# Optimization experiments

Hardware: AMD Instinct MI355X
Metric: run time of the kernel (lower is better)

The kernel has to match this reference:

```python
import jax, jax.numpy as jnp
import numpy as np
import math

H = 16        # num_heads
HD = 64       # head_dim


def get_slopes(n):
    def pow2(n):
        start = 2 ** (-2 ** (-(math.log2(n) - 3)))
        return [start * start ** i for i in range(n)]
    if math.log2(n).is_integer():
        return pow2(n)
    c = 2 ** math.floor(math.log2(n))
    return pow2(c) + get_slopes(2 * c)[0::2][: n - c]


def setup_inputs() -> dict:
    key = jax.random.key(0)
    ks = jax.random.split(key, 6)
    b, n, d = 2, 2048, 1024
    s = 1.0 / math.sqrt(d)
    return {
        "x": jax.random.normal(ks[0], (b, n, d), jnp.float32),
        "Wq": jax.random.normal(ks[1], (d, d), jnp.float32) * s,
        "Wk": jax.random.normal(ks[2], (d, d), jnp.float32) * s,
        "Wv": jax.random.normal(ks[3], (d, d), jnp.float32) * s,
        "Wo": jax.random.normal(ks[4], (d, d), jnp.float32) * s,
        "bo": jnp.zeros((d,), jnp.float32),
    }


def reference(x, Wq, Wk, Wv, Wo, bo):
    b, n, d = x.shape
    # project and split heads: [b, H, n, HD]
    def heads(w):
        return (x @ w).reshape(b, n, H, HD).transpose(0, 2, 1, 3)
    q, k, v = heads(Wq), heads(Wk), heads(Wv)

    scores = jnp.einsum("bhqd,bhkd->bhqk", q, k)  # [b,H,n,n]
    pos = jnp.arange(n)
    dist = jnp.abs(pos[None, :] - pos[:, None]).astype(scores.dtype)  # [n,n]
    slopes = jnp.asarray(get_slopes(H), dtype=scores.dtype)
    scores = scores - slopes[:, None, None] * dist  # alibi subtracted BEFORE scaling (as in source)
    causal = pos[None, :] > pos[:, None]            # upper triangle masked
    scores = jnp.where(causal, -jnp.inf, scores)
    attn = jax.nn.softmax(scores / math.sqrt(HD), axis=-1)
    ctx = jnp.einsum("bhqk,bhkd->bhqd", attn, v)
    ctx = ctx.transpose(0, 2, 1, 3).reshape(b, n, d)
    return ctx @ Wo + bo
```

## Files before the change

### kernel.cpp

```cpp
#include <hip/hip_runtime.h>
#include <hip/hip_bf16.h>
#include <stdint.h>

#define NH 16
#define HDIM 64
#define NB 2
#define NSEQ 2048
#define DM 1024
#define MROWS (NB * NSEQ)

typedef __attribute__((ext_vector_type(8))) short bf16x8;
typedef __attribute__((ext_vector_type(4))) float f32x4;

#define MFMA32(a, b, c) __builtin_amdgcn_mfma_f32_16x16x32_bf16(a, b, c, 0, 0, 0)

static __device__ __forceinline__ unsigned short f2bf(float f) {
    union { float f; unsigned u; } v;
    v.f = f;
    unsigned r = v.u + 0x7fffu + ((v.u >> 16) & 1u);
    return (unsigned short)(r >> 16);
}

static __device__ __forceinline__ unsigned pack2bf(float a, float b) {
#if __has_builtin(__builtin_amdgcn_cvt_pk_bf16_f32)
    typedef __attribute__((ext_vector_type(2))) __bf16 bf2_t;
    union { bf2_t v; unsigned u; } c;
    c.v = __builtin_amdgcn_cvt_pk_bf16_f32(a, b);
    return c.u;
#else
    return (unsigned)f2bf(a) | ((unsigned)f2bf(b) << 16);
#endif
}

static __device__ __forceinline__ float fexp2(float x) {
#if __has_builtin(__builtin_amdgcn_exp2f)
    return __builtin_amdgcn_exp2f(x);
#else
    return exp2f(x);
#endif
}

typedef __attribute__((address_space(1))) void* gas_ptr;
typedef __attribute__((address_space(3))) void* las_ptr;

static __device__ __forceinline__ void load16_lds(const void* g, void* l) {
    __builtin_amdgcn_global_load_lds((gas_ptr)(uintptr_t)g, (las_ptr)(uintptr_t)l,
                                     16, 0, 0);
}

__global__ __launch_bounds__(256) void convert_kernel(
    const float* __restrict__ x,
    const float* __restrict__ wq, const float* __restrict__ wk,
    const float* __restrict__ wv, const float* __restrict__ wo,
    unsigned short* __restrict__ xb,
    unsigned short* __restrict__ wqkvt,
    unsigned short* __restrict__ wot)
{
    __shared__ unsigned short Ts[64][66];
    int t = threadIdx.x;
    int bx = blockIdx.x;
    if (bx < 1024) {
        const float4* xs = (const float4*)x + (long)bx * 1024;
        unsigned short* xd = xb + (long)bx * 4096;
#pragma unroll
        for (int i = 0; i < 4; i++) {
            float4 v = xs[i * 256 + t];
            ushort4 o;
            o.x = f2bf(v.x); o.y = f2bf(v.y); o.z = f2bf(v.z); o.w = f2bf(v.w);
            *(ushort4*)(xd + (i * 256 + t) * 4) = o;
        }
        return;
    }
    int wi = bx - 1024;
    int wsel = wi >> 8;
    int tile = wi & 255;
    int k0 = (tile >> 4) * 64, c0 = (tile & 15) * 64;
    const float* w = (wsel == 0) ? wq : (wsel == 1) ? wk : (wsel == 2) ? wv : wo;
    int lr = t >> 6, lc = t & 63;
#pragma unroll
    for (int rr = 0; rr < 16; rr++) {
        int row = rr * 4 + lr;
        Ts[row][lc] = f2bf(w[(long)(k0 + row) * DM + c0 + lc]);
    }
    __syncthreads();
    unsigned short* dst = (wsel == 3) ? wot : (wqkvt + (long)wsel * DM * DM);
#pragma unroll
    for (int rr = 0; rr < 16; rr++) {
        int crow = rr * 4 + lr;
        dst[(long)(c0 + crow) * DM + k0 + lc] = Ts[lc][crow];
    }
}

static __device__ __forceinline__ void gemm_tile_128(
    const unsigned short* __restrict__ A, const unsigned short* __restrict__ Bt,
    int m0, int n0, unsigned short* As, unsigned short* Bs, f32x4 (&acc)[4][4])
{
    int t = threadIdx.x;
    int lane = t & 63;
    int wave = t >> 6;
    int l16 = lane & 15, quad = lane >> 4;
    int wm = wave >> 1, wn = wave & 1;

    int b0 = t, b1 = t + 256;
    int row0 = b0 >> 2, g0 = (b0 & 3) ^ ((row0 >> 1) & 3);
    int row1 = b1 >> 2, g1 = (b1 & 3) ^ ((row1 >> 1) & 3);
    const char* ga0 = (const char*)(A + (long)(m0 + row0) * DM) + g0 * 16;
    const char* ga1 = (const char*)(A + (long)(m0 + row1) * DM) + g1 * 16;
    const char* gb0 = (const char*)(Bt + (long)(n0 + row0) * DM) + g0 * 16;
    const char* gb1 = (const char*)(Bt + (long)(n0 + row1) * DM) + g1 * 16;
    char* sa0 = (char*)As + t * 16;
    char* sa1 = (char*)As + t * 16 + 4096;
    char* sb0 = (char*)Bs + t * 16;
    char* sb1 = (char*)Bs + t * 16 + 4096;

    int sread = quad ^ ((l16 >> 1) & 3);
    const unsigned short* fa = As + (wm * 64 + l16) * 32 + sread * 8;
    const unsigned short* fb = Bs + (wn * 64 + l16) * 32 + sread * 8;

    for (int kk = 0; kk < DM; kk += 32) {
        load16_lds(ga0 + kk * 2, sa0);
        load16_lds(ga1 + kk * 2, sa1);
        load16_lds(gb0 + kk * 2, sb0);
        load16_lds(gb1 + kk * 2, sb1);
        __syncthreads();
        bf16x8 af[4], bf[4];
#pragma unroll
        for (int r = 0; r < 4; r++) af[r] = *(const bf16x8*)(fa + r * 16 * 32);
#pragma unroll
        for (int c = 0; c < 4; c++) bf[c] = *(const bf16x8*)(fb + c * 16 * 32);
#pragma unroll
        for (int r = 0; r < 4; r++)
#pragma unroll
            for (int c = 0; c < 4; c++)
                acc[r][c] = MFMA32(af[r], bf[c], acc[r][c]);
        __syncthreads();
    }
}

__global__ __launch_bounds__(256) void qkv_gemm_kernel(
    const unsigned short* __restrict__ A,
    const unsigned short* __restrict__ Bt,
    unsigned short* __restrict__ Qo, unsigned short* __restrict__ Ko,
    unsigned short* __restrict__ Vt)
{
    __shared__ unsigned short As[128 * 32];
    __shared__ unsigned short Bs[128 * 32];
    __shared__ unsigned short Tw[4][16][72];

    f32x4 acc[4][4] = {};
    int m0 = blockIdx.y * 128, n0 = blockIdx.x * 128;
    gemm_tile_128(A, Bt, m0, n0, As, Bs, acc);

    int t = threadIdx.x, wave = t >> 6, lane = t & 63;
    int l16 = lane & 15, quad = lane >> 4;
    int wm = wave >> 1, wn = wave & 1;
    int rg0 = m0 + wm * 64;
    int cg0 = n0 + wn * 64;
    int z = cg0 >> 10;
    int b_ = rg0 >> 11;
    int nb0 = rg0 & (NSEQ - 1);
    int h = (cg0 & 1023) >> 6;
    long bh = (long)(b_ * NH + h);

    if (z < 2) {
        unsigned short* dst = (z == 0 ? Qo : Ko) + bh * NSEQ * HDIM;
#pragma unroll
        for (int r = 0; r < 4; r++)
#pragma unroll
            for (int reg = 0; reg < 4; reg++) {
                long rowb = (long)(nb0 + r * 16 + quad * 4 + reg) * HDIM;
#pragma unroll
                for (int c = 0; c < 4; c++)
                    dst[rowb + c * 16 + l16] = f2bf(acc[r][c][reg]);
            }
    } else {
        unsigned short* dst = Vt + bh * HDIM * NSEQ;
#pragma unroll
        for (int c = 0; c < 4; c++) {
#pragma unroll
            for (int r = 0; r < 4; r++) {
                ushort4 u;
                u.x = f2bf(acc[r][c][0]); u.y = f2bf(acc[r][c][1]);
                u.z = f2bf(acc[r][c][2]); u.w = f2bf(acc[r][c][3]);
                *(ushort4*)&Tw[wave][l16][r * 16 + quad * 4] = u;
            }
#pragma unroll
            for (int j = 0; j < 4; j++) {
                int lrow = j * 4 + quad;
                ushort4 u = *(const ushort4*)&Tw[wave][lrow][l16 * 4];
                *(ushort4*)(dst + (long)(c * 16 + lrow) * NSEQ + nb0 + l16 * 4) = u;
            }
        }
    }
}

static __device__ __forceinline__ void softmax_fixed(
    f32x4* s, bool mask, int qb, int kb, float sc2, float mrow,
    f32x4& l_vec, unsigned pbu[2][4], int l16, int quad)
{
    if (mask) {
        int fdm = qb + l16 - kb - quad * 4;
#pragma unroll
        for (int tt = 0; tt < 4; tt++)
#pragma unroll
            for (int r = 0; r < 4; r++)
                if (tt * 16 + r > fdm) s[tt][r] = -3e38f;
    }
    f32x4 e[4];
#pragma unroll
    for (int tt = 0; tt < 4; tt++)
#pragma unroll
        for (int r = 0; r < 4; r++)
            e[tt][r] = fexp2(s[tt][r] * sc2 - mrow);
#pragma unroll
    for (int r = 0; r < 4; r++)
        l_vec[r] += (e[0][r] + e[1][r]) + (e[2][r] + e[3][r]);

#pragma unroll
    for (int p = 0; p < 2; p++) {
        pbu[p][0] = pack2bf(e[2 * p][0],     e[2 * p][1]);
        pbu[p][1] = pack2bf(e[2 * p][2],     e[2 * p][3]);
        pbu[p][2] = pack2bf(e[2 * p + 1][0], e[2 * p + 1][1]);
        pbu[p][3] = pack2bf(e[2 * p + 1][2], e[2 * p + 1][3]);
    }
}

__global__ __launch_bounds__(512) void attn_kernel(
    const unsigned short* __restrict__ Q,
    const unsigned short* __restrict__ K,
    const unsigned short* __restrict__ Vt,
    unsigned short* __restrict__ ctx)
{
    __shared__ unsigned short KV[2][8192];

    int t = threadIdx.x, w = t >> 6, lane = t & 63;
    int l16 = lane & 15, quad = lane >> 4;
    int r7 = l16 & 7;
    int bh = blockIdx.x;
    int b_ = bh >> 4, h = bh & 15;
    int pr = blockIdx.y;
    int t1 = 31 - pr, t0 = pr;
    int nch = t1 + 1;
    bool isT0 = (w >= 4);
    int myTile = isT0 ? t0 : t1;
    int myNch = myTile + 1;
    int qb = myTile * 64 + (w & 3) * 16;

    const unsigned short* Kg  = K  + (long)bh * NSEQ * HDIM;
    const unsigned short* Vtg = Vt + (long)bh * HDIM * NSEQ;

    const float log2e = 1.44269504f;
    float slope = exp2f(-0.5f * (float)(h + 1));
    float sc2 = 0.125f * log2e;
    float ss2 = slope * sc2;

    const unsigned short* qp = Q + ((long)bh * NSEQ + qb + l16) * HDIM + quad * 8;
    bf16x8 aq0 = *(const bf16x8*)qp;
    bf16x8 aq1 = *(const bf16x8*)(qp + 32);

    f32x4 cinit[4];
#pragma unroll
    for (int tt = 0; tt < 4; tt++)
#pragma unroll
        for (int r = 0; r < 4; r++)
            cinit[tt][r] = slope * (float)(tt * 16 + quad * 4 + r);

    f32x4 lv = {};
    f32x4 o[4] = {};

    int row = t >> 3, sp = t & 7, sw = sp ^ (row & 7);
    const unsigned short* gk = Kg + row * HDIM + sw * 8;
    const unsigned short* gv = Vtg + (long)row * NSEQ + sw * 8;

    {
        unsigned short* buf = KV[0];
        load16_lds(gk, buf + t * 8);
        load16_lds(gv, buf + 4096 + t * 8);
    }

    for (int c = 0; c < nch; c++) {
        __syncthreads();
        if (c + 1 < nch) {
            int kb2 = (c + 1) * 64;
            unsigned short* buf = KV[(c + 1) & 1];
            load16_lds(gk + kb2 * HDIM, buf + t * 8);
            load16_lds(gv + kb2, buf + 4096 + t * 8);
        }
        if (isT0 && c >= myNch) continue;

        const unsigned short* Ks = KV[c & 1];
        const unsigned short* Vs = KV[c & 1] + 4096;
        int kb = c * 64;

        f32x4 s[4];
#pragma unroll
        for (int tt = 0; tt < 4; tt++) {
            int rr = tt * 16 + l16;
            bf16x8 k0 = *(const bf16x8*)(Ks + (rr * 8 + (quad ^ r7)) * 8);
            bf16x8 k1 = *(const bf16x8*)(Ks + (rr * 8 + ((quad + 4) ^ r7)) * 8);
            f32x4 z = MFMA32(k0, aq0, cinit[tt]);
            s[tt] = MFMA32(k1, aq1, z);
        }

        float mrow = ss2 * (float)(qb + l16 - kb);
        unsigned pb[2][4];
        softmax_fixed(s, c == myNch - 1, qb, kb, sc2, mrow, lv, pb, l16, quad);

        int q2 = quad >> 1, q1b = (quad & 1) << 3;
#pragma unroll
        for (int cb = 0; cb < 4; cb++) {
            int rd = cb * 16 + l16;
            const char* vrow = (const char*)(Vs + rd * 64);
            int x7 = rd & 7;
#pragma unroll
            for (int p = 0; p < 2; p++) {
                union { bf16x8 v; uint2 u2[2]; } a;
                int sb0 = 4 * p + q2;
                int sb1 = 4 * p + 2 + q2;
                a.u2[0] = *(const uint2*)(vrow + ((sb0 ^ x7) << 4) + q1b);
                a.u2[1] = *(const uint2*)(vrow + ((sb1 ^ x7) << 4) + q1b);
                union { unsigned u[4]; bf16x8 v; } bv;
#pragma unroll
                for (int i = 0; i < 4; i++) bv.u[i] = pb[p][i];
                o[cb] = MFMA32(a.v, bv.v, o[cb]);
            }
        }
    }

    {
        float lt = (lv[0] + lv[1]) + (lv[2] + lv[3]);
        lt += __shfl_xor(lt, 16);
        lt += __shfl_xor(lt, 32);
        float inv = 1.0f / lt;
        long base = (((long)b_ * NSEQ + (qb + l16)) * NH + h) * HDIM + quad * 4;
#pragma unroll
        for (int cb = 0; cb < 4; cb++) {
            uint2 u;
            u.x = pack2bf(o[cb][0] * inv, o[cb][1] * inv);
            u.y = pack2bf(o[cb][2] * inv, o[cb][3] * inv);
            *(uint2*)(ctx + base + cb * 16) = u;
        }
    }
}

__global__ __launch_bounds__(256) void out_gemm_kernel(
    const unsigned short* __restrict__ A,
    const unsigned short* __restrict__ Bt,
    const float* __restrict__ bias,
    float* __restrict__ out)
{
    __shared__ unsigned short As[128 * 32];
    __shared__ unsigned short Bs[128 * 32];
    f32x4 acc[4][4] = {};
    int m0 = blockIdx.y * 128, n0 = blockIdx.x * 128;
    gemm_tile_128(A, Bt, m0, n0, As, Bs, acc);

    int t = threadIdx.x, wave = t >> 6, lane = t & 63;
    int l16 = lane & 15, quad = lane >> 4;
    int wm = wave >> 1, wn = wave & 1;
    int rg0 = m0 + wm * 64, cg0 = n0 + wn * 64;
#pragma unroll
    for (int c = 0; c < 4; c++) {
        float bc = bias[cg0 + c * 16 + l16];
#pragma unroll
        for (int r = 0; r < 4; r++)
#pragma unroll
            for (int reg = 0; reg < 4; reg++)
                out[(long)(rg0 + r * 16 + quad * 4 + reg) * DM + cg0 + c * 16 + l16] =
                    acc[r][c][reg] + bc;
    }
}

extern "C" void kernel_launch(void* const* d_in, const int* in_sizes, int n_in,
                              void* d_out, int out_size, void* d_ws, size_t ws_size,
                              hipStream_t stream)
{
    const float* x  = (const float*)d_in[0];
    const float* wq = (const float*)d_in[1];
    const float* wk = (const float*)d_in[2];
    const float* wv = (const float*)d_in[3];
    const float* wo = (const float*)d_in[4];
    const float* bo = (const float*)d_in[5];

    char* ws = (char*)d_ws;
    unsigned short* xb    = (unsigned short*)(ws);
    unsigned short* wqkvt = (unsigned short*)(ws + (8L  << 20));
    unsigned short* wot   = (unsigned short*)(ws + (14L << 20));
    unsigned short* Qb    = (unsigned short*)(ws + (16L << 20));
    unsigned short* Kb    = (unsigned short*)(ws + (24L << 20));
    unsigned short* Vt    = (unsigned short*)(ws + (32L << 20));
    unsigned short* ctx   = (unsigned short*)(ws + (40L << 20));
    float* out = (float*)d_out;

    convert_kernel<<<2048, 256, 0, stream>>>(x, wq, wk, wv, wo, xb, wqkvt, wot);

    qkv_gemm_kernel<<<dim3(3 * DM / 128, MROWS / 128), 256, 0, stream>>>(
        xb, wqkvt, Qb, Kb, Vt);

    attn_kernel<<<dim3(NB * NH, 16), 512, 0, stream>>>(Qb, Kb, Vt, ctx);

    out_gemm_kernel<<<dim3(DM / 128, MROWS / 128), 256, 0, stream>>>(
        ctx, wot, bo, out);
}
```

Baseline: 186.6 us.

## Double-buffer LDS in GEMM tiles and halve output GEMM M tile

The GEMM core now keeps two LDS buffers and prefetches the next K slice while MFMAs run on the current one, which removes one barrier per iteration and overlaps global loads with compute. The output projection GEMM switches to 64x128 tiles so its grid doubles from 256 to 512 blocks and fills more CUs. The cost is twice the LDS per block, which may lower occupancy, plus less data reuse per output tile in the out GEMM.

```diff
diff --git a/kernel.cpp b/kernel.cpp
--- a/kernel.cpp
+++ b/kernel.cpp
@@ -91,49 +91,78 @@
     }
 }
 
-static __device__ __forceinline__ void gemm_tile_128(
-    const unsigned short* __restrict__ A, const unsigned short* __restrict__ Bt,
-    int m0, int n0, unsigned short* As, unsigned short* Bs, f32x4 (&acc)[4][4])
-{
+template<int MR>
+static __device__ __forceinline__ void gemm_core_db(
+    const unsigned short* __restrict__ A,
+    const unsigned short* __restrict__ Bt,
+    int m0, int n0,
+    unsigned short* __restrict__ As,
+    unsigned short* __restrict__ Bs,
+    f32x4 (&acc)[MR][4])
+{
+    constexpr int MT  = MR * 32;
+    constexpr int ASZ = MT * 32;
+    constexpr int BSZ = 128 * 32;
+    constexpr int NA  = MT / 64;
+
     int t = threadIdx.x;
     int lane = t & 63;
     int wave = t >> 6;
     int l16 = lane & 15, quad = lane >> 4;
     int wm = wave >> 1, wn = wave & 1;
 
-    int b0 = t, b1 = t + 256;
-    int row0 = b0 >> 2, g0 = (b0 & 3) ^ ((row0 >> 1) & 3);
-    int row1 = b1 >> 2, g1 = (b1 & 3) ^ ((row1 >> 1) & 3);
-    const char* ga0 = (const char*)(A + (long)(m0 + row0) * DM) + g0 * 16;
-    const char* ga1 = (const char*)(A + (long)(m0 + row1) * DM) + g1 * 16;
-    const char* gb0 = (const char*)(Bt + (long)(n0 + row0) * DM) + g0 * 16;
-    const char* gb1 = (const char*)(Bt + (long)(n0 + row1) * DM) + g1 * 16;
-    char* sa0 = (char*)As + t * 16;
-    char* sa1 = (char*)As + t * 16 + 4096;
-    char* sb0 = (char*)Bs + t * 16;
-    char* sb1 = (char*)Bs + t * 16 + 4096;
+    const char* gA[NA];
+#pragma unroll
+    for (int i = 0; i < NA; i++) {
+        int b = i * 256 + t;
+        int row = b >> 2, g = (b & 3) ^ ((row >> 1) & 3);
+        gA[i] = (const char*)(A + (long)(m0 + row) * DM) + g * 16;
+    }
+    const char* gB[2];
+#pragma unroll
+    for (int i = 0; i < 2; i++) {
+        int b = i * 256 + t;
+        int row = b >> 2, g = (b & 3) ^ ((row >> 1) & 3);
+        gB[i] = (const char*)(Bt + (long)(n0 + row) * DM) + g * 16;
+    }
 
     int sread = quad ^ ((l16 >> 1) & 3);
-    const unsigned short* fa = As + (wm * 64 + l16) * 32 + sread * 8;
-    const unsigned short* fb = Bs + (wn * 64 + l16) * 32 + sread * 8;
+    int faOff = (wm * (MT / 2) + l16) * 32 + sread * 8;
+    int fbOff = (wn * 64 + l16) * 32 + sread * 8;
+
+#pragma unroll
+    for (int i = 0; i < NA; i++)
+        load16_lds(gA[i], (char*)As + i * 4096 + t * 16);
+#pragma unroll
+    for (int i = 0; i < 2; i++)
+        load16_lds(gB[i], (char*)Bs + i * 4096 + t * 16);
 
     for (int kk = 0; kk < DM; kk += 32) {
-        load16_lds(ga0 + kk * 2, sa0);
-        load16_lds(ga1 + kk * 2, sa1);
-        load16_lds(gb0 + kk * 2, sb0);
-        load16_lds(gb1 + kk * 2, sb1);
+        int cur = (kk >> 5) & 1;
         __syncthreads();
-        bf16x8 af[4], bf[4];
-#pragma unroll
-        for (int r = 0; r < 4; r++) af[r] = *(const bf16x8*)(fa + r * 16 * 32);
+        if (kk + 32 < DM) {
+            int nxt = cur ^ 1;
+            char* abuf = (char*)(As + nxt * ASZ);
+            char* bbuf = (char*)(Bs + nxt * BSZ);
+#pragma unroll
+            for (int i = 0; i < NA; i++)
+                load16_lds(gA[i] + (kk + 32) * 2, abuf + i * 4096 + t * 16);
+#pragma unroll
+            for (int i = 0; i < 2; i++)
+                load16_lds(gB[i] + (kk + 32) * 2, bbuf + i * 4096 + t * 16);
+        }
+        const unsigned short* fa = As + cur * ASZ + faOff;
+        const unsigned short* fb = Bs + cur * BSZ + fbOff;
+        bf16x8 af[MR], bf[4];
+#pragma unroll
+        for (int r = 0; r < MR; r++) af[r] = *(const bf16x8*)(fa + r * 16 * 32);
 #pragma unroll
         for (int c = 0; c < 4; c++) bf[c] = *(const bf16x8*)(fb + c * 16 * 32);
 #pragma unroll
-        for (int r = 0; r < 4; r++)
+        for (int r = 0; r < MR; r++)
 #pragma unroll
             for (int c = 0; c < 4; c++)
                 acc[r][c] = MFMA32(af[r], bf[c], acc[r][c]);
-        __syncthreads();
     }
 }
 
@@ -143,13 +172,13 @@
     unsigned short* __restrict__ Qo, unsigned short* __restrict__ Ko,
     unsigned short* __restrict__ Vt)
 {
-    __shared__ unsigned short As[128 * 32];
-    __shared__ unsigned short Bs[128 * 32];
+    __shared__ unsigned short As[2][128 * 32];
+    __shared__ unsigned short Bs[2][128 * 32];
     __shared__ unsigned short Tw[4][16][72];
 
     f32x4 acc[4][4] = {};
     int m0 = blockIdx.y * 128, n0 = blockIdx.x * 128;
-    gemm_tile_128(A, Bt, m0, n0, As, Bs, acc);
+    gemm_core_db<4>(A, Bt, m0, n0, &As[0][0], &Bs[0][0], acc);
 
     int t = threadIdx.x, wave = t >> 6, lane = t & 63;
     int l16 = lane & 15, quad = lane >> 4;
@@ -349,21 +378,21 @@
     const float* __restrict__ bias,
     float* __restrict__ out)
 {
-    __shared__ unsigned short As[128 * 32];
-    __shared__ unsigned short Bs[128 * 32];
-    f32x4 acc[4][4] = {};
-    int m0 = blockIdx.y * 128, n0 = blockIdx.x * 128;
-    gemm_tile_128(A, Bt, m0, n0, As, Bs, acc);
+    __shared__ unsigned short As[2][64 * 32];
+    __shared__ unsigned short Bs[2][128 * 32];
+    f32x4 acc[2][4] = {};
+    int m0 = blockIdx.y * 64, n0 = blockIdx.x * 128;
+    gemm_core_db<2>(A, Bt, m0, n0, &As[0][0], &Bs[0][0], acc);
 
     int t = threadIdx.x, wave = t >> 6, lane = t & 63;
     int l16 = lane & 15, quad = lane >> 4;
     int wm = wave >> 1, wn = wave & 1;
-    int rg0 = m0 + wm * 64, cg0 = n0 + wn * 64;
+    int rg0 = m0 + wm * 32, cg0 = n0 + wn * 64;
 #pragma unroll
     for (int c = 0; c < 4; c++) {
         float bc = bias[cg0 + c * 16 + l16];
 #pragma unroll
-        for (int r = 0; r < 4; r++)
+        for (int r = 0; r < 2; r++)
 #pragma unroll
             for (int reg = 0; reg < 4; reg++)
                 out[(long)(rg0 + r * 16 + quad * 4 + reg) * DM + cg0 + c * 16 + l16] =
@@ -399,6 +428,6 @@
 
     attn_kernel<<<dim3(NB * NH, 16), 512, 0, stream>>>(Qb, Kb, Vt, ctx);
 
-    out_gemm_kernel<<<dim3(DM / 128, MROWS / 128), 256, 0, stream>>>(
+    out_gemm_kernel<<<dim3(DM / 128, MROWS / 64), 256, 0, stream>>>(
         ctx, wot, bo, out);
 }
```

After: 173.5 us. 7.0% less time.
